# Kernel tuning notes

Measured on AMD Instinct MI355X. Metric: run time of the kernel, lower is better.

The kernel has to match this reference:

```python
import jax, jax.numpy as jnp
import numpy as np
from math import comb

H, W = 256, 256          # canvas_shape
S = 15                   # num_samples along each bezier curve
EPS = 1e-6


def _bezier_samples(key_points):
    # key_points: [B, K, 2] in pixel coords. Uniform-t Bernstein evaluation.
    K = key_points.shape[1]
    ts = jnp.linspace(0.0, 1.0, S)                              # [S]
    k = jnp.arange(K)
    binom = jnp.asarray([comb(K - 1, i) for i in range(K)], dtype=key_points.dtype)
    basis = binom * ts[:, None] ** k * (1.0 - ts[:, None]) ** (K - 1 - k)  # [S, K]
    return jnp.einsum('sk,bkd->bsd', basis, key_points)         # [B, S, 2]


def setup_inputs() -> dict:
    key = jax.random.key(0)
    k1, k2, k3 = jax.random.split(key, 3)
    inputs = jax.random.uniform(k1, (64, 4, 2), dtype=jnp.float32)          # normalized (y, x)
    widths = jax.random.uniform(k2, (64,), dtype=jnp.float32) * 19.0 + 1.0  # 1..20 px
    aa_factors = jax.random.uniform(k3, (64,), dtype=jnp.float32) * 2.0 + 0.5
    return {"inputs": inputs, "widths": widths, "aa_factors": aa_factors}


def reference(inputs, widths, aa_factors):
    B = inputs.shape[0]
    canvas_shape = jnp.asarray([H, W], dtype=inputs.dtype)
    key_points = inputs * canvas_shape                 # [B, K, 2]
    sample_points = _bezier_samples(key_points)        # [B, S, 2]

    # positions built as [[y, x] for x in range(W) for y in range(H)] -> x-major flatten
    ys = jnp.tile(jnp.arange(H), W)
    xs = jnp.repeat(jnp.arange(W), H)
    positions = jnp.stack([ys, xs], axis=1).astype(inputs.dtype)   # [P, 2], P = H*W

    diff = positions[None, None, :, :] - sample_points[:, :, None, :]  # [B, S, P, 2]
    distances = jnp.sqrt(jnp.sum(diff * diff, axis=-1))                # [B, S, P]
    min_dist = jnp.min(distances, axis=1)                              # [B, P]

    canvas = (min_dist / widths[:, None] + EPS) ** aa_factors[:, None]
    canvas = jnp.clip(1.0 - canvas, 0.0, 1.0)
    return canvas.reshape(B, H, W)
```

## Files before the change

### kernel.cpp

```cpp
#include <hip/hip_runtime.h>

#define HH 256
#define WW 256
#define SS 15
#define NB 64

__device__ __forceinline__ float alog2(float x) {
    float r; asm("v_log_f32 %0, %1" : "=v"(r) : "v"(x)); return r;
}
__device__ __forceinline__ float aexp2(float x) {
    float r; asm("v_exp_f32 %0, %1" : "=v"(r) : "v"(x)); return r;
}

__global__ __launch_bounds__(256) void CurveGraphic2d_kernel(
    const float* __restrict__ inputs,
    const float* __restrict__ widths,
    const float* __restrict__ aaf,
    float* __restrict__ out)
{
    const int b     = blockIdx.x >> 6;
    const int chunk = blockIdx.x & 63;
    const int tid   = threadIdx.x;

    __shared__ float spy[SS];
    __shared__ float spx[SS];

    if (tid < SS) {
        float t = (float)tid * (1.0f / (float)(SS - 1));
        float u = 1.0f - t;
        float b0 = u * u * u;
        float b1 = 3.0f * t * u * u;
        float b2 = 3.0f * t * t * u;
        float b3 = t * t * t;
        const float* kp = inputs + b * 8;
        spy[tid] = 256.0f * (b0 * kp[0] + b1 * kp[2] + b2 * kp[4] + b3 * kp[6]);
        spx[tid] = 256.0f * (b0 * kp[1] + b1 * kp[3] + b2 * kp[5] + b3 * kp[7]);
    }
    __syncthreads();

    const float w  = widths[b];
    const float w2 = w * w;

    const int base = chunk * 1024 + tid * 4;
    const int i = base >> 8;
    const int j = base & 255;
    const float x  = (float)i;
    const float y0 = (float)j;

    float* dst = out + (size_t)b * (HH * WW) + base;

    float dxx[SS];
    float minv = 1e30f;
    #pragma unroll
    for (int s = 0; s < SS; ++s) {
        float dx = x - spx[s];
        dxx[s] = dx * dx;
        minv = fminf(minv, dxx[s]);
    }

    if (minv >= w2) {
        *reinterpret_cast<float4*>(dst) = make_float4(0.f, 0.f, 0.f, 0.f);
        return;
    }

    float m0 = 1e30f, m1 = 1e30f, m2 = 1e30f, m3 = 1e30f;
    #pragma unroll
    for (int s = 0; s < SS; ++s) {
        if (dxx[s] < w2) {
            float sy  = spy[s];
            float dy0 = y0          - sy;
            float dy1 = (y0 + 1.0f) - sy;
            float dy2 = (y0 + 2.0f) - sy;
            float dy3 = (y0 + 3.0f) - sy;
            m0 = fminf(m0, fmaf(dy0, dy0, dxx[s]));
            m1 = fminf(m1, fmaf(dy1, dy1, dxx[s]));
            m2 = fminf(m2, fmaf(dy2, dy2, dxx[s]));
            m3 = fminf(m3, fmaf(dy3, dy3, dxx[s]));
        }
    }

    const float af    = aaf[b];
    const float haf   = 0.5f * af;
    const float cbias = -af * log2f(w);

    float4 o;
    float p;
    p   = aexp2(fmaf(haf, alog2(m0), cbias));
    o.x = fminf(fmaxf(1.0f - p, 0.0f), 1.0f);
    p   = aexp2(fmaf(haf, alog2(m1), cbias));
    o.y = fminf(fmaxf(1.0f - p, 0.0f), 1.0f);
    p   = aexp2(fmaf(haf, alog2(m2), cbias));
    o.z = fminf(fmaxf(1.0f - p, 0.0f), 1.0f);
    p   = aexp2(fmaf(haf, alog2(m3), cbias));
    o.w = fminf(fmaxf(1.0f - p, 0.0f), 1.0f);

    *reinterpret_cast<float4*>(dst) = o;
}

extern "C" void kernel_launch(void* const* d_in, const int* in_sizes, int n_in,
                              void* d_out, int out_size, void* d_ws, size_t ws_size,
                              hipStream_t stream) {
    const float* inputs = (const float*)d_in[0];
    const float* widths = (const float*)d_in[1];
    const float* aaf    = (const float*)d_in[2];
    float* out = (float*)d_out;

    const int blocks = NB * ((HH * WW) / 1024);
    CurveGraphic2d_kernel<<<blocks, 256, 0, stream>>>(inputs, widths, aaf, out);
}
```

Baseline: 11.29 us.

## Broadcast curve samples via readlane and compute two rows per thread

Every wavefront now computes the Bezier samples per lane and broadcasts them with readlane, which removes the shared memory writes and the block barrier. Each thread covers two adjacent x rows with four y pixels each, so the dy squares are reused across both rows, and the grid is halved. The early all-zero exit is dropped, so far-away pixels now run the full loop and log/exp path, but the per-sample branch still skips inactive samples. Register pressure goes up, and wave-uniform readlane broadcasts replace LDS reads.

```diff
diff --git a/kernel.cpp b/kernel.cpp
--- a/kernel.cpp
+++ b/kernel.cpp
@@ -11,6 +11,9 @@
 __device__ __forceinline__ float aexp2(float x) {
     float r; asm("v_exp_f32 %0, %1" : "=v"(r) : "v"(x)); return r;
 }
+__device__ __forceinline__ float bcast(float v, int lane) {
+    return __uint_as_float(__builtin_amdgcn_readlane(__float_as_uint(v), lane));
+}
 
 __global__ __launch_bounds__(256) void CurveGraphic2d_kernel(
     const float* __restrict__ inputs,
@@ -18,64 +21,66 @@
     const float* __restrict__ aaf,
     float* __restrict__ out)
 {
-    const int b     = blockIdx.x >> 6;
-    const int chunk = blockIdx.x & 63;
-    const int tid   = threadIdx.x;
+    const int b    = blockIdx.x >> 5;
+    const int blk  = blockIdx.x & 31;
+    const int tid  = threadIdx.x;
+    const int lane = tid & 63;
+    const int r    = blk * 4 + (tid >> 6);
 
-    __shared__ float spy[SS];
-    __shared__ float spx[SS];
+    const float* kp = inputs + b * 8;
+    float t  = (float)lane * (1.0f / (float)(SS - 1));
+    float u  = 1.0f - t;
+    float b0 = u * u * u;
+    float b1 = 3.0f * t * u * u;
+    float b2 = 3.0f * t * t * u;
+    float b3 = t * t * t;
+    float spyv = 256.0f * (b0 * kp[0] + b1 * kp[2] + b2 * kp[4] + b3 * kp[6]);
+    float spxv = 256.0f * (b0 * kp[1] + b1 * kp[3] + b2 * kp[5] + b3 * kp[7]);
 
-    if (tid < SS) {
-        float t = (float)tid * (1.0f / (float)(SS - 1));
-        float u = 1.0f - t;
-        float b0 = u * u * u;
-        float b1 = 3.0f * t * u * u;
-        float b2 = 3.0f * t * t * u;
-        float b3 = t * t * t;
-        const float* kp = inputs + b * 8;
-        spy[tid] = 256.0f * (b0 * kp[0] + b1 * kp[2] + b2 * kp[4] + b3 * kp[6]);
-        spx[tid] = 256.0f * (b0 * kp[1] + b1 * kp[3] + b2 * kp[5] + b3 * kp[7]);
+    float sx[SS], sy[SS];
+    #pragma unroll
+    for (int s = 0; s < SS; ++s) {
+        sx[s] = bcast(spxv, s);
+        sy[s] = bcast(spyv, s);
     }
-    __syncthreads();
 
     const float w  = widths[b];
     const float w2 = w * w;
 
-    const int base = chunk * 1024 + tid * 4;
-    const int i = base >> 8;
-    const int j = base & 255;
-    const float x  = (float)i;
-    const float y0 = (float)j;
+    const float xA = (float)(r * 2);
+    const float xB = xA + 1.0f;
+    const float y0 = (float)(lane * 4);
 
-    float* dst = out + (size_t)b * (HH * WW) + base;
+    float mA0 = 1e30f, mA1 = 1e30f, mA2 = 1e30f, mA3 = 1e30f;
+    float mB0 = 1e30f, mB1 = 1e30f, mB2 = 1e30f, mB3 = 1e30f;
 
-    float dxx[SS];
-    float minv = 1e30f;
     #pragma unroll
     for (int s = 0; s < SS; ++s) {
-        float dx = x - spx[s];
-        dxx[s] = dx * dx;
-        minv = fminf(minv, dxx[s]);
-    }
-
-    if (minv >= w2) {
-        *reinterpret_cast<float4*>(dst) = make_float4(0.f, 0.f, 0.f, 0.f);
-        return;
-    }
-
-    float m0 = 1e30f, m1 = 1e30f, m2 = 1e30f, m3 = 1e30f;
-    #pragma unroll
-    for (int s = 0; s < SS; ++s) {
-        if (dxx[s] < w2) {
-            float sy  = spy[s];
-            float dy0 = y0          - sy;
-            float dy1 = (y0 + 1.0f) - sy;
-            float dy2 = (y0 + 2.0f) - sy;
-            float dy3 = (y0 + 3.0f) - sy;
-            m0 = fminf(m0, fmaf(dy0, dy0, dxx[s]));
-            m1 = fminf(m1, fmaf(dy1, dy1, dxx[s]));
-            m2 = fminf(m2, fmaf(dy2, dy2, dxx[s]));
-            m3 = fminf(m3, fmaf(dy3, dy3, dxx[s]));
+        float dxA  = xA - sx[s];
+        float dxxA = dxA * dxA;
+        float dxB  = xB - sx[s];
+        float dxxB = dxB * dxB;
+        bool aA = dxxA < w2;
+        bool aB = dxxB < w2;
+        if (aA || aB) {
+            float sys = sy[s];
+            float dy0 = y0          - sys;
+            float dy1 = (y0 + 1.0f) - sys;
+            float dy2 = (y0 + 2.0f) - sys;
+            float dy3 = (y0 + 3.0f) - sys;
+            float q0 = dy0 * dy0, q1 = dy1 * dy1, q2 = dy2 * dy2, q3 = dy3 * dy3;
+            if (aA) {
+                mA0 = fminf(mA0, q0 + dxxA);
+                mA1 = fminf(mA1, q1 + dxxA);
+                mA2 = fminf(mA2, q2 + dxxA);
+                mA3 = fminf(mA3, q3 + dxxA);
+            }
+            if (aB) {
+                mB0 = fminf(mB0, q0 + dxxB);
+                mB1 = fminf(mB1, q1 + dxxB);
+                mB2 = fminf(mB2, q2 + dxxB);
+                mB3 = fminf(mB3, q3 + dxxB);
+            }
         }
     }
 
@@ -83,18 +88,29 @@
     const float haf   = 0.5f * af;
     const float cbias = -af * log2f(w);
 
+    float* dst = out + (size_t)b * (HH * WW) + r * 512 + lane * 4;
+
     float4 o;
     float p;
-    p   = aexp2(fmaf(haf, alog2(m0), cbias));
+    p   = aexp2(fmaf(haf, alog2(mA0), cbias));
     o.x = fminf(fmaxf(1.0f - p, 0.0f), 1.0f);
-    p   = aexp2(fmaf(haf, alog2(m1), cbias));
+    p   = aexp2(fmaf(haf, alog2(mA1), cbias));
     o.y = fminf(fmaxf(1.0f - p, 0.0f), 1.0f);
-    p   = aexp2(fmaf(haf, alog2(m2), cbias));
+    p   = aexp2(fmaf(haf, alog2(mA2), cbias));
     o.z = fminf(fmaxf(1.0f - p, 0.0f), 1.0f);
-    p   = aexp2(fmaf(haf, alog2(m3), cbias));
+    p   = aexp2(fmaf(haf, alog2(mA3), cbias));
     o.w = fminf(fmaxf(1.0f - p, 0.0f), 1.0f);
+    *reinterpret_cast<float4*>(dst) = o;
 
-    *reinterpret_cast<float4*>(dst) = o;
+    p   = aexp2(fmaf(haf, alog2(mB0), cbias));
+    o.x = fminf(fmaxf(1.0f - p, 0.0f), 1.0f);
+    p   = aexp2(fmaf(haf, alog2(mB1), cbias));
+    o.y = fminf(fmaxf(1.0f - p, 0.0f), 1.0f);
+    p   = aexp2(fmaf(haf, alog2(mB2), cbias));
+    o.z = fminf(fmaxf(1.0f - p, 0.0f), 1.0f);
+    p   = aexp2(fmaf(haf, alog2(mB3), cbias));
+    o.w = fminf(fmaxf(1.0f - p, 0.0f), 1.0f);
+    *reinterpret_cast<float4*>(dst + 256) = o;
 }
 
 extern "C" void kernel_launch(void* const* d_in, const int* in_sizes, int n_in,
@@ -105,6 +121,6 @@
     const float* aaf    = (const float*)d_in[2];
     float* out = (float*)d_out;
 
-    const int blocks = NB * ((HH * WW) / 1024);
+    const int blocks = NB * 32;
     CurveGraphic2d_kernel<<<blocks, 256, 0, stream>>>(inputs, widths, aaf, out);
 }
```

Result: slower. 12.19 us (+8.0%).
